# Performance work log

Measured on AMD Instinct MI355X. Metric: run time of the kernel, lower is better.

Reference implementation:

```python
import jax, jax.numpy as jnp
import numpy as np

LAMBDA = 0.01  # sparsity_threshold
SCALE = 0.02
NUM_BLOCKS = 4


def setup_inputs() -> dict:
    key = jax.random.key(0)
    k1, k2, k3, k4, k5 = jax.random.split(key, 5)
    B, N, C = 8, 4096, 512
    bs = C // NUM_BLOCKS
    return {
        "x": jax.random.normal(k1, (B, N, C), dtype=jnp.float32),
        "w1": jax.random.normal(k2, (2, NUM_BLOCKS, bs, bs), dtype=jnp.float32) * SCALE,
        "w2": jax.random.normal(k3, (2, NUM_BLOCKS, bs, bs), dtype=jnp.float32) * SCALE,
        "b1": jax.random.normal(k4, (2, NUM_BLOCKS, bs), dtype=jnp.float32) * SCALE,
        "b2": jax.random.normal(k5, (2, NUM_BLOCKS, bs), dtype=jnp.float32) * SCALE,
        "H": 64,
        "W": 64,
    }


def _softshrink(v):
    return jnp.where(v > LAMBDA, v - LAMBDA, jnp.where(v < -LAMBDA, v + LAMBDA, jnp.zeros((), v.dtype)))


def reference(x, w1, w2, b1, b2, H, W):
    B, N, C = x.shape
    bs = C // NUM_BLOCKS
    xb = x.reshape(B, N, NUM_BLOCKS, bs)
    # FFT over (token, block) axes, ortho norm — faithful to torch fft2(dim=(1,2))
    xf = jnp.fft.fft2(xb, axes=(1, 2), norm="ortho")
    re, im = jnp.real(xf), jnp.imag(xf)

    mul = lambda a, w: jnp.einsum("tnbd,bdk->tnbk", a, w)  # block-diagonal matmul

    r1 = jax.nn.relu(mul(re, w1[0]) - mul(im, w1[1]) + b1[0])
    i1 = jax.nn.relu(mul(re, w1[1]) + mul(im, w1[0]) + b1[1])
    r2 = mul(r1, w2[0]) - mul(i1, w2[1]) + b2[0]
    i2 = mul(r1, w2[1]) + mul(i1, w2[0]) + b2[1]

    z = _softshrink(r2) + 1j * _softshrink(i2)
    out = jnp.real(jnp.fft.ifft2(z, axes=(1, 2), norm="ortho"))  # .to(float32) keeps real part
    return out.reshape(B, N, C).astype(jnp.float32)
```

## Files before the change

kernel.cpp:

```cpp
#include <hip/hip_runtime.h>
#include <math.h>

#define TWO_PI 6.283185307179586f

typedef __attribute__((ext_vector_type(8))) short bf16x8;
typedef __attribute__((ext_vector_type(4))) short bf16x4;
typedef __attribute__((ext_vector_type(4))) float f32x4;
typedef __attribute__((ext_vector_type(4))) _Float16 h16x4;
typedef __attribute__((ext_vector_type(8))) _Float16 h16x8;

__device__ __forceinline__ short f2bf(float f) {
    unsigned u = __float_as_uint(f);
    unsigned r = (u + 0x7FFFu + ((u >> 16) & 1u)) >> 16;
    return (short)r;
}
__device__ __forceinline__ float bf2f(short s) {
    return __uint_as_float(((unsigned)(unsigned short)s) << 16);
}

__device__ __forceinline__ int dr4(int s) {
    return ((s & 3) << 4) | (s & 12) | ((s >> 4) & 3);
}

__device__ __forceinline__ void cmulw(float& xr, float& xi, float wr, float wi) {
    const float tr = xr * wr - xi * wi;
    xi = xr * wi + xi * wr;
    xr = tr;
}

__device__ __forceinline__ f32x4 ld4bf(const char* Z, int off) {
    const bf16x4 v = *(const bf16x4*)(Z + off);
    f32x4 r;
    r[0] = bf2f(v[0]); r[1] = bf2f(v[1]); r[2] = bf2f(v[2]); r[3] = bf2f(v[3]);
    return r;
}
__device__ __forceinline__ void st4bf(char* Z, int off, f32x4 a) {
    bf16x4 v;
    v[0] = f2bf(a[0]); v[1] = f2bf(a[1]); v[2] = f2bf(a[2]); v[3] = f2bf(a[3]);
    *(bf16x4*)(Z + off) = v;
}

#define DECODE_BCT() \
    const int b  = blockIdx.x >> 8; \
    const int dg = (blockIdx.x >> 2) & 63; \
    const int ct = blockIdx.x & 3;

#define GADDR(slot, blk, f4) \
    (((size_t)(b * 4096 + (slot)) * 512) + (size_t)((blk) * 128 + ct * 32 + (f4) * 4))

#define SETUP_TABLE48() \
    if (tid < 48) { \
        float s_, c_; \
        sincosf(TWO_PI * (float)tid / 64.0f, &s_, &c_); \
        wre[tid] = c_; wim[tid] = -s_; \
    }

__device__ __forceinline__ void dif_stage_A(char* Z, const float* wtr, const float* wti,
                                            int cg, int h, int s) {
    const int q  = 16 >> (2 * s);
    const int tw = 1 << (2 * s);
    const int j = h & (q - 1);
    const int g = (s == 0) ? 0 : (h >> (4 - 2 * s));
    const int i0 = g * (q << 2) + j;
    const int i1 = i0 + q, i2 = i1 + q, i3 = i2 + q;
    const int cbR = cg * 8, cbI = cbR + 256;
    const int oR0 = i0 * 512 + (cbR ^ ((i0 & 7) << 4)), oI0 = i0 * 512 + (cbI ^ ((i0 & 7) << 4));
    const int oR1 = i1 * 512 + (cbR ^ ((i1 & 7) << 4)), oI1 = i1 * 512 + (cbI ^ ((i1 & 7) << 4));
    const int oR2 = i2 * 512 + (cbR ^ ((i2 & 7) << 4)), oI2 = i2 * 512 + (cbI ^ ((i2 & 7) << 4));
    const int oR3 = i3 * 512 + (cbR ^ ((i3 & 7) << 4)), oI3 = i3 * 512 + (cbI ^ ((i3 & 7) << 4));
    const f32x4 a0r = ld4bf(Z, oR0), a0i = ld4bf(Z, oI0);
    const f32x4 a1r = ld4bf(Z, oR1), a1i = ld4bf(Z, oI1);
    const f32x4 a2r = ld4bf(Z, oR2), a2i = ld4bf(Z, oI2);
    const f32x4 a3r = ld4bf(Z, oR3), a3i = ld4bf(Z, oI3);
    const int m = j * tw;
    const float w1r = wtr[m],     w1i = wti[m];
    const float w2r = wtr[2 * m], w2i = wti[2 * m];
    const float w3r = wtr[3 * m], w3i = wti[3 * m];
    f32x4 O0r, O0i, O1r, O1i, O2r, O2i, O3r, O3i;
#pragma unroll
    for (int e = 0; e < 4; ++e) {
        const float t0r = a0r[e] + a2r[e], t0i = a0i[e] + a2i[e];
        const float t2r = a0r[e] - a2r[e], t2i = a0i[e] - a2i[e];
        const float t1r = a1r[e] + a3r[e], t1i = a1i[e] + a3i[e];
        const float dr  = a1r[e] - a3r[e], di  = a1i[e] - a3i[e];
        const float t3r = di, t3i = -dr;
        O0r[e] = t0r + t1r;  O0i[e] = t0i + t1i;
        float y1r = t2r + t3r, y1i = t2i + t3i;
        float y2r = t0r - t1r, y2i = t0i - t1i;
        float y3r = t2r - t3r, y3i = t2i - t3i;
        if (m) {
            cmulw(y1r, y1i, w1r, w1i);
            cmulw(y2r, y2i, w2r, w2i);
            cmulw(y3r, y3i, w3r, w3i);
        }
        O1r[e] = y1r; O1i[e] = y1i;
        O2r[e] = y2r; O2i[e] = y2i;
        O3r[e] = y3r; O3i[e] = y3i;
    }
    st4bf(Z, oR0, O0r);  st4bf(Z, oI0, O0i);
    st4bf(Z, oR1, O1r);  st4bf(Z, oI1, O1i);
    st4bf(Z, oR2, O2r);  st4bf(Z, oI2, O2i);
    st4bf(Z, oR3, O3r);  st4bf(Z, oI3, O3i);
}

__device__ __forceinline__ void dit_stage_A(char* Z, const float* wtr, const float* wti,
                                            int cg, int h, int s) {
    const int q  = 16 >> (2 * s);
    const int tw = 1 << (2 * s);
    const int j = h & (q - 1);
    const int g = (s == 0) ? 0 : (h >> (4 - 2 * s));
    const int i0 = g * (q << 2) + j;
    const int i1 = i0 + q, i2 = i1 + q, i3 = i2 + q;
    const int cbR = cg * 8, cbI = cbR + 256;
    const int oR0 = i0 * 512 + (cbR ^ ((i0 & 7) << 4)), oI0 = i0 * 512 + (cbI ^ ((i0 & 7) << 4));
    const int oR1 = i1 * 512 + (cbR ^ ((i1 & 7) << 4)), oI1 = i1 * 512 + (cbI ^ ((i1 & 7) << 4));
    const int oR2 = i2 * 512 + (cbR ^ ((i2 & 7) << 4)), oI2 = i2 * 512 + (cbI ^ ((i2 & 7) << 4));
    const int oR3 = i3 * 512 + (cbR ^ ((i3 & 7) << 4)), oI3 = i3 * 512 + (cbI ^ ((i3 & 7) << 4));
    const f32x4 a0r = ld4bf(Z, oR0), a0i = ld4bf(Z, oI0);
    const f32x4 a1r = ld4bf(Z, oR1), a1i = ld4bf(Z, oI1);
    const f32x4 a2r = ld4bf(Z, oR2), a2i = ld4bf(Z, oI2);
    const f32x4 a3r = ld4bf(Z, oR3), a3i = ld4bf(Z, oI3);
    const int m = j * tw;
    const float w1r = wtr[m],     w1i = -wti[m];
    const float w2r = wtr[2 * m], w2i = -wti[2 * m];
    const float w3r = wtr[3 * m], w3i = -wti[3 * m];
    f32x4 O0r, O0i, O1r, O1i, O2r, O2i, O3r, O3i;
#pragma unroll
    for (int e = 0; e < 4; ++e) {
        float b1r = a1r[e], b1i = a1i[e];
        float b2r = a2r[e], b2i = a2i[e];
        float b3r = a3r[e], b3i = a3i[e];
        if (m) {
            cmulw(b1r, b1i, w1r, w1i);
            cmulw(b2r, b2i, w2r, w2i);
            cmulw(b3r, b3i, w3r, w3i);
        }
        const float u0r = a0r[e] + b2r, u0i = a0i[e] + b2i;
        const float u1r = a0r[e] - b2r, u1i = a0i[e] - b2i;
        const float u2r = b1r + b3r,    u2i = b1i + b3i;
        const float dr  = b1r - b3r,    di  = b1i - b3i;
        const float u3r = -di, u3i = dr;
        O0r[e] = u0r + u2r; O0i[e] = u0i + u2i;
        O1r[e] = u1r + u3r; O1i[e] = u1i + u3i;
        O2r[e] = u0r - u2r; O2i[e] = u0i - u2i;
        O3r[e] = u1r - u3r; O3i[e] = u1i - u3i;
    }
    st4bf(Z, oR0, O0r);  st4bf(Z, oI0, O0i);
    st4bf(Z, oR1, O1r);  st4bf(Z, oI1, O1i);
    st4bf(Z, oR2, O2r);  st4bf(Z, oI2, O2i);
    st4bf(Z, oR3, O3r);  st4bf(Z, oI3, O3i);
}

template<int W>
__device__ __forceinline__ void fft64_dif4v(_Float16 (*Lre)[W], _Float16 (*Lim)[W],
                                            const float* wtr, const float* wti,
                                            int c4, int h) {
#pragma unroll
    for (int s = 0; s < 3; ++s) {
        const int q  = 16 >> (2 * s);
        const int tw = 1 << (2 * s);
        __syncthreads();
        const int j = h & (q - 1);
        const int g = (s == 0) ? 0 : (h >> (4 - 2 * s));
        const int i0 = g * (q << 2) + j;
        const int i1 = i0 + q, i2 = i1 + q, i3 = i2 + q;
        const h16x4 A0r = *(const h16x4*)&Lre[i0][c4], A0i = *(const h16x4*)&Lim[i0][c4];
        const h16x4 A1r = *(const h16x4*)&Lre[i1][c4], A1i = *(const h16x4*)&Lim[i1][c4];
        const h16x4 A2r = *(const h16x4*)&Lre[i2][c4], A2i = *(const h16x4*)&Lim[i2][c4];
        const h16x4 A3r = *(const h16x4*)&Lre[i3][c4], A3i = *(const h16x4*)&Lim[i3][c4];
        const int m = j * tw;
        const float w1r = wtr[m],     w1i = wti[m];
        const float w2r = wtr[2 * m], w2i = wti[2 * m];
        const float w3r = wtr[3 * m], w3i = wti[3 * m];
        h16x4 O0r, O0i, O1r, O1i, O2r, O2i, O3r, O3i;
#pragma unroll
        for (int e = 0; e < 4; ++e) {
            const float a0r = (float)A0r[e], a0i = (float)A0i[e];
            const float a1r = (float)A1r[e], a1i = (float)A1i[e];
            const float a2r = (float)A2r[e], a2i = (float)A2i[e];
            const float a3r = (float)A3r[e], a3i = (float)A3i[e];
            const float t0r = a0r + a2r, t0i = a0i + a2i;
            const float t2r = a0r - a2r, t2i = a0i - a2i;
            const float t1r = a1r + a3r, t1i = a1i + a3i;
            const float dr  = a1r - a3r, di  = a1i - a3i;
            const float t3r = di, t3i = -dr;
            O0r[e] = (_Float16)(t0r + t1r);  O0i[e] = (_Float16)(t0i + t1i);
            float y1r = t2r + t3r, y1i = t2i + t3i;
            float y2r = t0r - t1r, y2i = t0i - t1i;
            float y3r = t2r - t3r, y3i = t2i - t3i;
            if (m) {
                cmulw(y1r, y1i, w1r, w1i);
                cmulw(y2r, y2i, w2r, w2i);
                cmulw(y3r, y3i, w3r, w3i);
            }
            O1r[e] = (_Float16)y1r; O1i[e] = (_Float16)y1i;
            O2r[e] = (_Float16)y2r; O2i[e] = (_Float16)y2i;
            O3r[e] = (_Float16)y3r; O3i[e] = (_Float16)y3i;
        }
        *(h16x4*)&Lre[i0][c4] = O0r;  *(h16x4*)&Lim[i0][c4] = O0i;
        *(h16x4*)&Lre[i1][c4] = O1r;  *(h16x4*)&Lim[i1][c4] = O1i;
        *(h16x4*)&Lre[i2][c4] = O2r;  *(h16x4*)&Lim[i2][c4] = O2i;
        *(h16x4*)&Lre[i3][c4] = O3r;  *(h16x4*)&Lim[i3][c4] = O3i;
    }
    __syncthreads();
}

template<int W>
__device__ __forceinline__ void fft64_dit4v(_Float16 (*Lre)[W], _Float16 (*Lim)[W],
                                            const float* wtr, const float* wti,
                                            int c4, int h) {
#pragma unroll
    for (int s = 2; s >= 0; --s) {
        const int q  = 16 >> (2 * s);
        const int tw = 1 << (2 * s);
        __syncthreads();
        const int j = h & (q - 1);
        const int g = (s == 0) ? 0 : (h >> (4 - 2 * s));
        const int i0 = g * (q << 2) + j;
        const int i1 = i0 + q, i2 = i1 + q, i3 = i2 + q;
        const h16x4 A0r = *(const h16x4*)&Lre[i0][c4], A0i = *(const h16x4*)&Lim[i0][c4];
        const h16x4 A1r = *(const h16x4*)&Lre[i1][c4], A1i = *(const h16x4*)&Lim[i1][c4];
        const h16x4 A2r = *(const h16x4*)&Lre[i2][c4], A2i = *(const h16x4*)&Lim[i2][c4];
        const h16x4 A3r = *(const h16x4*)&Lre[i3][c4], A3i = *(const h16x4*)&Lim[i3][c4];
        const int m = j * tw;
        const float w1r = wtr[m],     w1i = -wti[m];
        const float w2r = wtr[2 * m], w2i = -wti[2 * m];
        const float w3r = wtr[3 * m], w3i = -wti[3 * m];
        h16x4 O0r, O0i, O1r, O1i, O2r, O2i, O3r, O3i;
#pragma unroll
        for (int e = 0; e < 4; ++e) {
            float b1r = (float)A1r[e], b1i = (float)A1i[e];
            float b2r = (float)A2r[e], b2i = (float)A2i[e];
            float b3r = (float)A3r[e], b3i = (float)A3i[e];
            if (m) {
                cmulw(b1r, b1i, w1r, w1i);
                cmulw(b2r, b2i, w2r, w2i);
                cmulw(b3r, b3i, w3r, w3i);
            }
            const float a0r = (float)A0r[e], a0i = (float)A0i[e];
            const float u0r = a0r + b2r, u0i = a0i + b2i;
            const float u1r = a0r - b2r, u1i = a0i - b2i;
            const float u2r = b1r + b3r, u2i = b1i + b3i;
            const float dr  = b1r - b3r, di  = b1i - b3i;
            const float u3r = -di, u3i = dr;
            O0r[e] = (_Float16)(u0r + u2r); O0i[e] = (_Float16)(u0i + u2i);
            O1r[e] = (_Float16)(u1r + u3r); O1i[e] = (_Float16)(u1i + u3i);
            O2r[e] = (_Float16)(u0r - u2r); O2i[e] = (_Float16)(u0i - u2i);
            O3r[e] = (_Float16)(u1r - u3r); O3i[e] = (_Float16)(u1i - u3i);
        }
        *(h16x4*)&Lre[i0][c4] = O0r;  *(h16x4*)&Lim[i0][c4] = O0i;
        *(h16x4*)&Lre[i1][c4] = O1r;  *(h16x4*)&Lim[i1][c4] = O1i;
        *(h16x4*)&Lre[i2][c4] = O2r;  *(h16x4*)&Lim[i2][c4] = O2i;
        *(h16x4*)&Lre[i3][c4] = O3r;  *(h16x4*)&Lim[i3][c4] = O3i;
    }
    __syncthreads();
}

extern "C" __global__ void __launch_bounds__(512)
fft_fwd_a(const float* __restrict__ x, short* __restrict__ zre, short* __restrict__ zim) {
    __shared__ __align__(16) _Float16 Lre[64][136];
    __shared__ __align__(16) _Float16 Lim[64][136];
    __shared__ float wre[48], wim[48];
    __shared__ float twr[64], twi[64];
    const int tid = threadIdx.x;
    SETUP_TABLE48();
    DECODE_BCT();
    if (tid >= 64 && tid < 128) {
        const int s1 = tid - 64;
        float sn, cs;
        sincosf(-(TWO_PI / 4096.0f) * (float)(dg * dr4(s1)), &sn, &cs);
        twr[s1] = cs; twi[s1] = sn;
    }
    for (int idx = tid; idx < 2048; idx += 512) {
        const int n1 = idx >> 5, q = idx & 31, blk = q >> 3, f4 = q & 7;
        const int cl = blk * 32 + f4 * 4;
        const float4 v = *(const float4*)(x + GADDR(n1 * 64 + dg, blk, f4));
        h16x4 hv, hz;
        hv[0] = (_Float16)v.x; hv[1] = (_Float16)v.y;
        hv[2] = (_Float16)v.z; hv[3] = (_Float16)v.w;
        hz[0] = (_Float16)0.f; hz[1] = (_Float16)0.f;
        hz[2] = (_Float16)0.f; hz[3] = (_Float16)0.f;
        *(h16x4*)&Lre[n1][cl] = hv;
        *(h16x4*)&Lim[n1][cl] = hz;
    }
    fft64_dif4v<136>(Lre, Lim, wre, wim, (tid & 31) * 4, tid >> 5);
    {
        const int s1 = tid >> 3, f4 = tid & 7;
        const float cs = twr[s1], sn = twi[s1];
        f32x4 r[4], m[4];
#pragma unroll
        for (int blk = 0; blk < 4; ++blk) {
            const int cl = blk * 32 + f4 * 4;
            const h16x4 hr = *(const h16x4*)&Lre[s1][cl];
            const h16x4 hi = *(const h16x4*)&Lim[s1][cl];
#pragma unroll
            for (int e = 0; e < 4; ++e) {
                const float vr = (float)hr[e], vi = (float)hi[e];
                r[blk][e] = vr * cs - vi * sn;
                m[blk][e] = vr * sn + vi * cs;
            }
        }
        const float sc = 1.0f / 128.0f;
        f32x4 yr[4], ym[4];
#pragma unroll
        for (int e = 0; e < 4; ++e) {
            const float r0 = r[0][e], r1 = r[1][e], r2 = r[2][e], r3 = r[3][e];
            const float m0 = m[0][e], m1 = m[1][e], m2 = m[2][e], m3 = m[3][e];
            yr[0][e] = (r0 + r1 + r2 + r3) * sc;  ym[0][e] = (m0 + m1 + m2 + m3) * sc;
            yr[1][e] = (r0 + m1 - r2 - m3) * sc;  ym[1][e] = (m0 - r1 - m2 + r3) * sc;
            yr[2][e] = (r0 - r1 + r2 - r3) * sc;  ym[2][e] = (m0 - m1 + m2 - m3) * sc;
            yr[3][e] = (r0 - m1 - r2 + m3) * sc;  ym[3][e] = (m0 + r1 - m2 - r3) * sc;
        }
#pragma unroll
        for (int blk = 0; blk < 4; ++blk) {
            bf16x4 pr, pi;
#pragma unroll
            for (int e = 0; e < 4; ++e) {
                pr[e] = f2bf(yr[blk][e]);
                pi[e] = f2bf(ym[blk][e]);
            }
            const size_t g = GADDR(s1 * 64 + dg, blk, f4);
            *(bf16x4*)(zre + g) = pr;
            *(bf16x4*)(zim + g) = pi;
        }
    }
}

extern "C" __global__ void __launch_bounds__(512)
fft_inv_b(const short* __restrict__ zre, const short* __restrict__ zim,
          float* __restrict__ out) {
    __shared__ __align__(16) _Float16 Lre[64][136];
    __shared__ __align__(16) _Float16 Lim[64][136];
    __shared__ float wre[48], wim[48];
    __shared__ float twr[64], twi[64];
    const int tid = threadIdx.x;
    SETUP_TABLE48();
    DECODE_BCT();
    if (tid >= 64 && tid < 128) {
        const int s1 = tid - 64;
        float sn, cs;
        sincosf((TWO_PI / 4096.0f) * (float)(dg * dr4(s1)), &sn, &cs);
        twr[s1] = cs; twi[s1] = sn;
    }
    __syncthreads();
    {
        const int s1 = tid >> 3, f4 = tid & 7;
        const float cs = twr[s1], sn = twi[s1];
        f32x4 r[4], m[4];
#pragma unroll
        for (int blk = 0; blk < 4; ++blk) {
            const size_t g = GADDR(s1 * 64 + dg, blk, f4);
            const bf16x4 vr = *(const bf16x4*)(zre + g);
            const bf16x4 vi = *(const bf16x4*)(zim + g);
#pragma unroll
            for (int e = 0; e < 4; ++e) {
                const float ar = bf2f(vr[e]), ai = bf2f(vi[e]);
                r[blk][e] = ar * cs - ai * sn;
                m[blk][e] = ar * sn + ai * cs;
            }
        }
        const float sc = 1.0f / 128.0f;
        f32x4 yr[4], ym[4];
#pragma unroll
        for (int e = 0; e < 4; ++e) {
            const float r0 = r[0][e], r1 = r[1][e], r2 = r[2][e], r3 = r[3][e];
            const float m0 = m[0][e], m1 = m[1][e], m2 = m[2][e], m3 = m[3][e];
            yr[0][e] = (r0 + r1 + r2 + r3) * sc;  ym[0][e] = (m0 + m1 + m2 + m3) * sc;
            yr[1][e] = (r0 - m1 - r2 + m3) * sc;  ym[1][e] = (m0 + r1 - m2 - r3) * sc;
            yr[2][e] = (r0 - r1 + r2 - r3) * sc;  ym[2][e] = (m0 - m1 + m2 - m3) * sc;
            yr[3][e] = (r0 + m1 - r2 - m3) * sc;  ym[3][e] = (m0 - r1 - m2 + r3) * sc;
        }
#pragma unroll
        for (int blk = 0; blk < 4; ++blk) {
            const int cl = blk * 32 + f4 * 4;
            h16x4 hr, hi;
#pragma unroll
            for (int e = 0; e < 4; ++e) {
                hr[e] = (_Float16)yr[blk][e];
                hi[e] = (_Float16)ym[blk][e];
            }
            *(h16x4*)&Lre[s1][cl] = hr;
            *(h16x4*)&Lim[s1][cl] = hi;
        }
    }
    fft64_dit4v<136>(Lre, Lim, wre, wim, (tid & 31) * 4, tid >> 5);
    for (int idx = tid; idx < 2048; idx += 512) {
        const int n1 = idx >> 5, q = idx & 31, blk = q >> 3, f4 = q & 7;
        const int cl = blk * 32 + f4 * 4;
        const h16x4 hr = *(const h16x4*)&Lre[n1][cl];
        float4 o;
        o.x = (float)hr[0]; o.y = (float)hr[1];
        o.z = (float)hr[2]; o.w = (float)hr[3];
        *(float4*)(out + GADDR(n1 * 64 + dg, blk, f4)) = o;
    }
}

extern "C" __global__ void __launch_bounds__(256)
wprep(const float* __restrict__ w1, const float* __restrict__ w2,
      short* __restrict__ wb) {
    const int i4  = blockIdx.x * 256 + threadIdx.x;
    const int k0  = (i4 & 63) * 4;
    const int n   = (i4 >> 6) & 255;
    const int blk = (i4 >> 14) & 3;
    const int L   = i4 >> 16;
    const float* w = L ? w2 : w1;
    bf16x4 pv;
#pragma unroll
    for (int j = 0; j < 4; ++j) {
        const int k = k0 + j;
        float v;
        if (k < 128) {
            v = (n < 128) ? w[blk * 16384 + k * 128 + n]
                          : w[65536 + blk * 16384 + k * 128 + (n - 128)];
        } else {
            v = (n < 128) ? -w[65536 + blk * 16384 + (k - 128) * 128 + n]
                          :  w[blk * 16384 + (k - 128) * 128 + (n - 128)];
        }
        pv[j] = f2bf(v);
    }
    *(bf16x4*)(wb + (size_t)i4 * 4) = pv;
}

#define MITER 4

__device__ __forceinline__ void stage_tile(const short* __restrict__ zre,
                                           const short* __restrict__ zim,
                                           char* Abuf, int rowbase, int blk,
                                           int wave, int lane) {
#pragma unroll
    for (int it = 0; it < 4; ++it) {
        const int chunk = wave * 256 + it * 64 + lane;
        const int row   = chunk >> 5;
        const unsigned kbyte = ((unsigned)((chunk & 31) << 4)) ^ ((unsigned)((row & 7) << 4));
        const int k0 = (int)(kbyte >> 1);
        const short* src = (k0 < 128) ? zre : zim;
        const size_t g = (size_t)(rowbase + row) * 512 + blk * 128 + (k0 & 127);
        unsigned* lp = (unsigned*)(Abuf + (wave * 4096 + it * 1024));
        __builtin_amdgcn_global_load_lds((const unsigned*)(src + g), lp, 16, 0, 0);
    }
}

template<int LAYER>
__global__ void __launch_bounds__(512)
mlp_fused(short* __restrict__ zre, short* __restrict__ zim,
          const short* __restrict__ wb, const float* __restrict__ bias) {
    __shared__ __align__(16) char As[2][64 * 256 * 2];
    __shared__ float wre[48], wim[48];

    const int blk  = blockIdx.y;
    const int tid  = threadIdx.x;
    const int wave = tid >> 6;
    const int lane = tid & 63;
    const int lrow = lane & 15;
    const int lk   = lane >> 4;
    const int cg   = tid & 31;
    const int fh   = tid >> 5;
    SETUP_TABLE48();

    bf16x8 Bf[2][8];
#pragma unroll
    for (int nt = 0; nt < 2; ++nt) {
        const int n = wave * 32 + nt * 16 + lrow;
#pragma unroll
        for (int ks = 0; ks < 8; ++ks) {
            Bf[nt][ks] = *(const bf16x8*)(wb + ((size_t)(blk * 256 + n) * 256 + ks * 32 + lk * 8));
        }
    }

    f32x4 bv4[2];
#pragma unroll
    for (int nt = 0; nt < 2; ++nt) {
        const int n0 = wave * 32 + nt * 16 + lk * 4;
        const float* bp = bias + ((n0 < 128) ? (blk * 128 + n0)
                                             : (512 + blk * 128 + (n0 - 128)));
        bv4[nt] = *(const f32x4*)bp;
    }

    stage_tile(zre, zim, As[0], blockIdx.x * MITER * 64, blk, wave, lane);

    for (int t = 0; t < MITER; ++t) {
        __syncthreads();

        char* Ab = As[t & 1];
        const int rowbase = (blockIdx.x * MITER + t) * 64;

        if (LAYER == 1) {
            dif_stage_A(Ab, wre, wim, cg, fh, 0);
            __syncthreads();
            dif_stage_A(Ab, wre, wim, cg, fh, 1);
            __syncthreads();
            dif_stage_A(Ab, wre, wim, cg, fh, 2);
            __syncthreads();
        }

        if (t + 1 < MITER)
            stage_tile(zre, zim, As[(t + 1) & 1],
                       (blockIdx.x * MITER + t + 1) * 64, blk, wave, lane);

        f32x4 acc[4][2];
#pragma unroll
        for (int mt = 0; mt < 4; ++mt)
#pragma unroll
            for (int nt = 0; nt < 2; ++nt)
                acc[mt][nt] = (f32x4){0.f, 0.f, 0.f, 0.f};

#pragma unroll
        for (int ks = 0; ks < 8; ++ks) {
            bf16x8 af[4];
#pragma unroll
            for (int mt = 0; mt < 4; ++mt) {
                const int row = mt * 16 + lrow;
                const int k0  = ks * 32 + lk * 8;
                const unsigned byteoff =
                    ((unsigned)(row * 512 + k0 * 2)) ^ ((unsigned)((row & 7) << 4));
                af[mt] = *(const bf16x8*)(Ab + byteoff);
            }
#pragma unroll
            for (int mt = 0; mt < 4; ++mt)
#pragma unroll
                for (int nt = 0; nt < 2; ++nt)
                    acc[mt][nt] = __builtin_amdgcn_mfma_f32_16x16x32_bf16(
                        Bf[nt][ks], af[mt], acc[mt][nt], 0, 0, 0);
        }

        if (LAYER == 1) {
#pragma unroll
            for (int nt = 0; nt < 2; ++nt) {
                const int n0 = wave * 32 + nt * 16 + lk * 4;
                short* dst = (n0 < 128) ? zre : zim;
                const int colb = blk * 128 + (n0 & 127);
#pragma unroll
                for (int mt = 0; mt < 4; ++mt) {
                    const int row = rowbase + mt * 16 + lrow;
                    bf16x4 pv;
#pragma unroll
                    for (int r = 0; r < 4; ++r)
                        pv[r] = f2bf(fmaxf(acc[mt][nt][r] + bv4[nt][r], 0.0f));
                    *(bf16x4*)(dst + (size_t)row * 512 + colb) = pv;
                }
            }
        } else {
            __syncthreads();
#pragma unroll
            for (int nt = 0; nt < 2; ++nt) {
                const int n0 = wave * 32 + nt * 16 + lk * 4;
                const int cb = n0 * 2;
#pragma unroll
                for (int mt = 0; mt < 4; ++mt) {
                    const int row = mt * 16 + lrow;
                    bf16x4 pv;
#pragma unroll
                    for (int r = 0; r < 4; ++r) {
                        float v = acc[mt][nt][r] + bv4[nt][r];
                        v = (v > 0.01f) ? v - 0.01f : ((v < -0.01f) ? v + 0.01f : 0.0f);
                        pv[r] = f2bf(v);
                    }
                    *(bf16x4*)(Ab + row * 512 + (cb ^ ((row & 7) << 4))) = pv;
                }
            }
            __syncthreads();
            dit_stage_A(Ab, wre, wim, cg, fh, 2);
            __syncthreads();
            dit_stage_A(Ab, wre, wim, cg, fh, 1);
            __syncthreads();
            dit_stage_A(Ab, wre, wim, cg, fh, 0);
            __syncthreads();
#pragma unroll
            for (int kk = 0; kk < 4; ++kk) {
                const int idx = tid + kk * 512;
                const int row = idx >> 5;
                const int q = idx & 31;
                const int p = q >> 4;
                const int c = q & 15;
                const int cbyte = p * 256 + c * 16;
                const bf16x8 v = *(const bf16x8*)(Ab + row * 512 + (cbyte ^ ((row & 7) << 4)));
                short* dst = p ? zim : zre;
                *(bf16x8*)(dst + (size_t)(rowbase + row) * 512 + blk * 128 + c * 8) = v;
            }
        }
    }
}

extern "C" void kernel_launch(void* const* d_in, const int* in_sizes, int n_in,
                              void* d_out, int out_size, void* d_ws, size_t ws_size,
                              hipStream_t stream) {
    const float* x  = (const float*)d_in[0];
    const float* w1 = (const float*)d_in[1];
    const float* w2 = (const float*)d_in[2];
    const float* b1 = (const float*)d_in[3];
    const float* b2 = (const float*)d_in[4];

    float* out = (float*)d_out;
    short* zre = (short*)d_ws;
    short* zim = zre + 16777216;
    short* wb  = (short*)d_out;
    const size_t WB_L = 4ull * 256 * 256;

    wprep<<<512, 256, 0, stream>>>(w1, w2, wb);

    fft_fwd_a<<<2048, 512, 0, stream>>>(x, zre, zim);

    mlp_fused<1><<<dim3(32768 / (64 * MITER), 4), 512, 0, stream>>>(zre, zim, wb, b1);
    mlp_fused<2><<<dim3(32768 / (64 * MITER), 4), 512, 0, stream>>>(zre, zim, wb + WB_L, b2);

    fft_inv_b<<<2048, 512, 0, stream>>>(zre, zim, out);
}
```

Baseline: 193.3 us.

## Fuse both MLP layers into one kernel keeping hidden activations in LDS

Merges the two per-layer MLP kernels into a single kernel. The layer-1 ReLU output is written back into the shared-memory tile and consumed directly by the layer-2 matmul, so it no longer makes a global memory round trip and one launch disappears. To keep register pressure manageable, weight fragments are now reloaded from global/L2 for each tile and each layer instead of being held in registers for the whole kernel. The launch bound now requests 4 blocks per multiprocessor, and extra barriers are added between the layers.

Result: slower. 379.3 us (+96.3%).

```diff
diff --git a/kernel.cpp b/kernel.cpp
--- a/kernel.cpp
+++ b/kernel.cpp
@@ -440,10 +440,10 @@
     }
 }
 
-template<int LAYER>
-__global__ void __launch_bounds__(512)
-mlp_fused(short* __restrict__ zre, short* __restrict__ zim,
-          const short* __restrict__ wb, const float* __restrict__ bias) {
+extern "C" __global__ void __launch_bounds__(512, 4)
+mlp_both(short* __restrict__ zre, short* __restrict__ zim,
+         const short* __restrict__ wb,
+         const float* __restrict__ b1g, const float* __restrict__ b2g) {
     __shared__ __align__(16) char As[2][64 * 256 * 2];
     __shared__ float wre[48], wim[48];
 
@@ -457,23 +457,13 @@
     const int fh   = tid >> 5;
     SETUP_TABLE48();
 
-    bf16x8 Bf[2][8];
-#pragma unroll
-    for (int nt = 0; nt < 2; ++nt) {
-        const int n = wave * 32 + nt * 16 + lrow;
-#pragma unroll
-        for (int ks = 0; ks < 8; ++ks) {
-            Bf[nt][ks] = *(const bf16x8*)(wb + ((size_t)(blk * 256 + n) * 256 + ks * 32 + lk * 8));
-        }
-    }
-
-    f32x4 bv4[2];
+    f32x4 bv1[2], bv2[2];
 #pragma unroll
     for (int nt = 0; nt < 2; ++nt) {
         const int n0 = wave * 32 + nt * 16 + lk * 4;
-        const float* bp = bias + ((n0 < 128) ? (blk * 128 + n0)
-                                             : (512 + blk * 128 + (n0 - 128)));
-        bv4[nt] = *(const f32x4*)bp;
+        const int bi = (n0 < 128) ? (blk * 128 + n0) : (512 + blk * 128 + (n0 - 128));
+        bv1[nt] = *(const f32x4*)(b1g + bi);
+        bv2[nt] = *(const f32x4*)(b2g + bi);
     }
 
     stage_tile(zre, zim, As[0], blockIdx.x * MITER * 64, blk, wave, lane);
@@ -484,99 +474,142 @@
         char* Ab = As[t & 1];
         const int rowbase = (blockIdx.x * MITER + t) * 64;
 
-        if (LAYER == 1) {
-            dif_stage_A(Ab, wre, wim, cg, fh, 0);
-            __syncthreads();
-            dif_stage_A(Ab, wre, wim, cg, fh, 1);
-            __syncthreads();
-            dif_stage_A(Ab, wre, wim, cg, fh, 2);
-            __syncthreads();
-        }
+        dif_stage_A(Ab, wre, wim, cg, fh, 0);
+        __syncthreads();
+        dif_stage_A(Ab, wre, wim, cg, fh, 1);
+        __syncthreads();
+        dif_stage_A(Ab, wre, wim, cg, fh, 2);
+        __syncthreads();
 
         if (t + 1 < MITER)
             stage_tile(zre, zim, As[(t + 1) & 1],
                        (blockIdx.x * MITER + t + 1) * 64, blk, wave, lane);
 
         f32x4 acc[4][2];
-#pragma unroll
-        for (int mt = 0; mt < 4; ++mt)
-#pragma unroll
-            for (int nt = 0; nt < 2; ++nt)
-                acc[mt][nt] = (f32x4){0.f, 0.f, 0.f, 0.f};
-
-#pragma unroll
-        for (int ks = 0; ks < 8; ++ks) {
-            bf16x8 af[4];
+
+        {
+            bf16x8 Bf[2][8];
+#pragma unroll
+            for (int nt = 0; nt < 2; ++nt) {
+                const int n = wave * 32 + nt * 16 + lrow;
+#pragma unroll
+                for (int ks = 0; ks < 8; ++ks)
+                    Bf[nt][ks] = *(const bf16x8*)(wb +
+                        ((size_t)(blk * 256 + n) * 256 + ks * 32 + lk * 8));
+            }
+#pragma unroll
+            for (int mt = 0; mt < 4; ++mt)
+#pragma unroll
+                for (int nt = 0; nt < 2; ++nt)
+                    acc[mt][nt] = (f32x4){0.f, 0.f, 0.f, 0.f};
+#pragma unroll
+            for (int ks = 0; ks < 8; ++ks) {
+                bf16x8 af[4];
+#pragma unroll
+                for (int mt = 0; mt < 4; ++mt) {
+                    const int row = mt * 16 + lrow;
+                    const int k0  = ks * 32 + lk * 8;
+                    const unsigned byteoff =
+                        ((unsigned)(row * 512 + k0 * 2)) ^ ((unsigned)((row & 7) << 4));
+                    af[mt] = *(const bf16x8*)(Ab + byteoff);
+                }
+#pragma unroll
+                for (int mt = 0; mt < 4; ++mt)
+#pragma unroll
+                    for (int nt = 0; nt < 2; ++nt)
+                        acc[mt][nt] = __builtin_amdgcn_mfma_f32_16x16x32_bf16(
+                            Bf[nt][ks], af[mt], acc[mt][nt], 0, 0, 0);
+            }
+        }
+        __syncthreads();
+#pragma unroll
+        for (int nt = 0; nt < 2; ++nt) {
+            const int n0 = wave * 32 + nt * 16 + lk * 4;
+            const int cb = n0 * 2;
 #pragma unroll
             for (int mt = 0; mt < 4; ++mt) {
                 const int row = mt * 16 + lrow;
-                const int k0  = ks * 32 + lk * 8;
-                const unsigned byteoff =
-                    ((unsigned)(row * 512 + k0 * 2)) ^ ((unsigned)((row & 7) << 4));
-                af[mt] = *(const bf16x8*)(Ab + byteoff);
+                bf16x4 pv;
+#pragma unroll
+                for (int r = 0; r < 4; ++r)
+                    pv[r] = f2bf(fmaxf(acc[mt][nt][r] + bv1[nt][r], 0.0f));
+                *(bf16x4*)(Ab + row * 512 + (cb ^ ((row & 7) << 4))) = pv;
+            }
+        }
+        __syncthreads();
+
+        {
+            bf16x8 Bf[2][8];
+#pragma unroll
+            for (int nt = 0; nt < 2; ++nt) {
+                const int n = wave * 32 + nt * 16 + lrow;
+#pragma unroll
+                for (int ks = 0; ks < 8; ++ks)
+                    Bf[nt][ks] = *(const bf16x8*)(wb + 262144 +
+                        ((size_t)(blk * 256 + n) * 256 + ks * 32 + lk * 8));
             }
 #pragma unroll
             for (int mt = 0; mt < 4; ++mt)
 #pragma unroll
                 for (int nt = 0; nt < 2; ++nt)
-                    acc[mt][nt] = __builtin_amdgcn_mfma_f32_16x16x32_bf16(
-                        Bf[nt][ks], af[mt], acc[mt][nt], 0, 0, 0);
-        }
-
-        if (LAYER == 1) {
-#pragma unroll
-            for (int nt = 0; nt < 2; ++nt) {
-                const int n0 = wave * 32 + nt * 16 + lk * 4;
-                short* dst = (n0 < 128) ? zre : zim;
-                const int colb = blk * 128 + (n0 & 127);
-#pragma unroll
-                for (int mt = 0; mt < 4; ++mt) {
-                    const int row = rowbase + mt * 16 + lrow;
-                    bf16x4 pv;
-#pragma unroll
-                    for (int r = 0; r < 4; ++r)
-                        pv[r] = f2bf(fmaxf(acc[mt][nt][r] + bv4[nt][r], 0.0f));
-                    *(bf16x4*)(dst + (size_t)row * 512 + colb) = pv;
-                }
-            }
-        } else {
-            __syncthreads();
-#pragma unroll
-            for (int nt = 0; nt < 2; ++nt) {
-                const int n0 = wave * 32 + nt * 16 + lk * 4;
-                const int cb = n0 * 2;
+                    acc[mt][nt] = (f32x4){0.f, 0.f, 0.f, 0.f};
+#pragma unroll
+            for (int ks = 0; ks < 8; ++ks) {
+                bf16x8 af[4];
 #pragma unroll
                 for (int mt = 0; mt < 4; ++mt) {
                     const int row = mt * 16 + lrow;
-                    bf16x4 pv;
-#pragma unroll
-                    for (int r = 0; r < 4; ++r) {
-                        float v = acc[mt][nt][r] + bv4[nt][r];
-                        v = (v > 0.01f) ? v - 0.01f : ((v < -0.01f) ? v + 0.01f : 0.0f);
-                        pv[r] = f2bf(v);
-                    }
-                    *(bf16x4*)(Ab + row * 512 + (cb ^ ((row & 7) << 4))) = pv;
+                    const int k0  = ks * 32 + lk * 8;
+                    const unsigned byteoff =
+                        ((unsigned)(row * 512 + k0 * 2)) ^ ((unsigned)((row & 7) << 4));
+                    af[mt] = *(const bf16x8*)(Ab + byteoff);
                 }
-            }
-            __syncthreads();
-            dit_stage_A(Ab, wre, wim, cg, fh, 2);
-            __syncthreads();
-            dit_stage_A(Ab, wre, wim, cg, fh, 1);
-            __syncthreads();
-            dit_stage_A(Ab, wre, wim, cg, fh, 0);
-            __syncthreads();
-#pragma unroll
-            for (int kk = 0; kk < 4; ++kk) {
-                const int idx = tid + kk * 512;
-                const int row = idx >> 5;
-                const int q = idx & 31;
-                const int p = q >> 4;
-                const int c = q & 15;
-                const int cbyte = p * 256 + c * 16;
-                const bf16x8 v = *(const bf16x8*)(Ab + row * 512 + (cbyte ^ ((row & 7) << 4)));
-                short* dst = p ? zim : zre;
-                *(bf16x8*)(dst + (size_t)(rowbase + row) * 512 + blk * 128 + c * 8) = v;
-            }
+#pragma unroll
+                for (int mt = 0; mt < 4; ++mt)
+#pragma unroll
+                    for (int nt = 0; nt < 2; ++nt)
+                        acc[mt][nt] = __builtin_amdgcn_mfma_f32_16x16x32_bf16(
+                            Bf[nt][ks], af[mt], acc[mt][nt], 0, 0, 0);
+            }
+        }
+        __syncthreads();
+#pragma unroll
+        for (int nt = 0; nt < 2; ++nt) {
+            const int n0 = wave * 32 + nt * 16 + lk * 4;
+            const int cb = n0 * 2;
+#pragma unroll
+            for (int mt = 0; mt < 4; ++mt) {
+                const int row = mt * 16 + lrow;
+                bf16x4 pv;
+#pragma unroll
+                for (int r = 0; r < 4; ++r) {
+                    float v = acc[mt][nt][r] + bv2[nt][r];
+                    v = (v > 0.01f) ? v - 0.01f : ((v < -0.01f) ? v + 0.01f : 0.0f);
+                    pv[r] = f2bf(v);
+                }
+                *(bf16x4*)(Ab + row * 512 + (cb ^ ((row & 7) << 4))) = pv;
+            }
+        }
+        __syncthreads();
+
+        dit_stage_A(Ab, wre, wim, cg, fh, 2);
+        __syncthreads();
+        dit_stage_A(Ab, wre, wim, cg, fh, 1);
+        __syncthreads();
+        dit_stage_A(Ab, wre, wim, cg, fh, 0);
+        __syncthreads();
+
+#pragma unroll
+        for (int kk = 0; kk < 4; ++kk) {
+            const int idx = tid + kk * 512;
+            const int row = idx >> 5;
+            const int q = idx & 31;
+            const int p = q >> 4;
+            const int c = q & 15;
+            const int cbyte = p * 256 + c * 16;
+            const bf16x8 v = *(const bf16x8*)(Ab + row * 512 + (cbyte ^ ((row & 7) << 4)));
+            short* dst = p ? zim : zre;
+            *(bf16x8*)(dst + (size_t)(rowbase + row) * 512 + blk * 128 + c * 8) = v;
         }
     }
 }
@@ -594,14 +627,12 @@
     short* zre = (short*)d_ws;
     short* zim = zre + 16777216;
     short* wb  = (short*)d_out;
-    const size_t WB_L = 4ull * 256 * 256;
 
     wprep<<<512, 256, 0, stream>>>(w1, w2, wb);
 
     fft_fwd_a<<<2048, 512, 0, stream>>>(x, zre, zim);
 
-    mlp_fused<1><<<dim3(32768 / (64 * MITER), 4), 512, 0, stream>>>(zre, zim, wb, b1);
-    mlp_fused<2><<<dim3(32768 / (64 * MITER), 4), 512, 0, stream>>>(zre, zim, wb + WB_L, b2);
+    mlp_both<<<dim3(32768 / (64 * MITER), 4), 512, 0, stream>>>(zre, zim, wb, b1, b2);
 
     fft_inv_b<<<2048, 512, 0, stream>>>(zre, zim, out);
 }
```
